# Kernel tuning notes

Hardware: AMD Instinct MI355X
Metric: run time of the kernel (lower is better)

Reference implementation:

```python
import jax, jax.numpy as jnp
import numpy as np

B, T, C = 2, 2048, 2048
N_HEAD = 16
N_KV = 4
HEAD = C // N_HEAD  # 128
GROUP = N_HEAD // N_KV


def setup_inputs() -> dict:
    key = jax.random.key(0)
    ks = jax.random.split(key, 5)
    s = 1.0 / np.sqrt(C)
    return {
        "x": jax.random.normal(ks[0], (B, T, C), dtype=jnp.float32),
        "Wq": jax.random.normal(ks[1], (C, C), dtype=jnp.float32) * s,
        "Wk": jax.random.normal(ks[2], (C, N_KV * HEAD), dtype=jnp.float32) * s,
        "Wv": jax.random.normal(ks[3], (C, N_KV * HEAD), dtype=jnp.float32) * s,
        "Wo": jax.random.normal(ks[4], (C, C), dtype=jnp.float32) * s,
    }


def reference(x, Wq, Wk, Wv, Wo):
    Bx, Tx, Cx = x.shape
    q = (x @ Wq).reshape(Bx, Tx, N_HEAD, HEAD).transpose(0, 2, 1, 3)  # (B,H,T,D)
    k = (x @ Wk).reshape(Bx, Tx, N_KV, HEAD).transpose(0, 2, 1, 3)    # (B,KV,T,D)
    v = (x @ Wv).reshape(Bx, Tx, N_KV, HEAD).transpose(0, 2, 1, 3)
    # expand kv heads to query heads (GQA): repeat each kv head GROUP times
    k = jnp.repeat(k, GROUP, axis=1)  # (B,H,T,D)
    v = jnp.repeat(v, GROUP, axis=1)
    scale = 1.0 / np.sqrt(HEAD).astype(np.float32)
    att = jnp.einsum("bhqd,bhkd->bhqk", q, k) * scale  # (B,H,T,T)
    causal = jnp.tril(jnp.ones((Tx, Tx), dtype=bool))
    att = jnp.where(causal[None, None], att, -jnp.inf)
    att = jax.nn.softmax(att, axis=-1)
    y = jnp.einsum("bhqk,bhkd->bhqd", att, v)  # (B,H,T,D)
    y = y.transpose(0, 2, 1, 3).reshape(Bx, Tx, Cx)
    return y @ Wo
```

## Files before the change

kernel.cpp:

```cpp
#include <hip/hip_runtime.h>
#include <cstdint>

typedef unsigned short u16;
typedef unsigned int u32;
typedef __attribute__((ext_vector_type(8))) __bf16 bf16x8;
typedef __attribute__((ext_vector_type(4))) float f32x4;
typedef __attribute__((ext_vector_type(4))) unsigned short u16x4;

#define AS1 __attribute__((address_space(1)))
#define AS3 __attribute__((address_space(3)))

__device__ __forceinline__ void gload16(const void* g, void* l) {
    __builtin_amdgcn_global_load_lds((AS1 void*)g, (AS3 void*)l, 16, 0, 0);
}

__device__ __forceinline__ u16 f2bf(float f) {
    return __builtin_bit_cast(u16, (__bf16)f);
}

__device__ __forceinline__ void store_c(u16* p, float v)   { *p = f2bf(v); }
__device__ __forceinline__ void store_c(float* p, float v) { *p = v; }

__global__ void prep(const float* __restrict__ x,
                     const float* __restrict__ Wq, const float* __restrict__ Wk,
                     const float* __restrict__ Wv, const float* __restrict__ Wo,
                     u16* __restrict__ xb, u16* __restrict__ Wt)
{
    const int bid = blockIdx.x;
    if (bid >= 10240) {
        int tid = threadIdx.y * 32 + threadIdx.x;
        size_t i = ((size_t)(bid - 10240) * 256 + tid) * 4;
        float4 v = *(const float4*)(x + i);
        u16x4 o = { f2bf(v.x), f2bf(v.y), f2bf(v.z), f2bf(v.w) };
        *(u16x4*)(xb + i) = o;
        return;
    }
    const float* src; u16* dst; int C, bx, by;
    if (bid < 4096)      { src = Wq; dst = Wt;                          C = 2048; bx = bid & 63; by = bid >> 6; }
    else if (bid < 5120) { src = Wk; dst = Wt + (size_t)2048 * 2048;    C = 512;  int i = bid - 4096; bx = i & 15; by = i >> 4; }
    else if (bid < 6144) { src = Wv; dst = Wt + (size_t)2560 * 2048;    C = 512;  int i = bid - 5120; bx = i & 15; by = i >> 4; }
    else                 { src = Wo; dst = Wt + (size_t)3072 * 2048;    C = 2048; int i = bid - 6144; bx = i & 63; by = i >> 6; }
    __shared__ float tile[32][33];
    int c0 = bx * 32, r0 = by * 32;
    int tx = threadIdx.x, ty = threadIdx.y;
#pragma unroll
    for (int i = 0; i < 32; i += 8)
        tile[ty + i][tx] = src[(size_t)(r0 + ty + i) * C + c0 + tx];
    __syncthreads();
#pragma unroll
    for (int i = 0; i < 32; i += 8)
        dst[(size_t)(c0 + ty + i) * 2048 + r0 + tx] = f2bf(tile[tx][ty + i]);
}

__global__ void vtrans(const u16* __restrict__ QKV, u16* __restrict__ VT) {
    __shared__ u16 tile[32][33];
    int b = blockIdx.z;
    int c0 = blockIdx.x * 32, r0 = blockIdx.y * 32;
    int tx = threadIdx.x, ty = threadIdx.y;
#pragma unroll
    for (int i = 0; i < 32; i += 8)
        tile[ty + i][tx] = QKV[(size_t)(b * 2048 + r0 + ty + i) * 3072 + 2560 + c0 + tx];
    __syncthreads();
#pragma unroll
    for (int i = 0; i < 32; i += 8)
        VT[(size_t)(b * 512 + c0 + ty + i) * 2048 + r0 + tx] = tile[tx][ty + i];
}

template <typename OT>
__global__ __launch_bounds__(256, 2) void gemm_bt(
    const u16* __restrict__ A, const u16* __restrict__ Bt,
    OT* __restrict__ C, int M, int N, int K)
{
    __shared__ u16 As[128 * 64];
    __shared__ u16 Bs[128 * 64];
    const int tid  = threadIdx.x;
    const int wave = tid >> 6, lane = tid & 63;
    const int quad = lane >> 4, l15 = lane & 15;
    const int bm0 = blockIdx.y * 128, bn0 = blockIdx.x * 128;
    const int wr = (wave >> 1) * 64, wc = (wave & 1) * 64;

    const f32x4 zero = {0.f, 0.f, 0.f, 0.f};
    f32x4 acc[4][4];
#pragma unroll
    for (int i = 0; i < 4; ++i)
#pragma unroll
        for (int j = 0; j < 4; ++j) acc[i][j] = zero;

    const int srow = lane >> 3;
    const int jsw  = ((lane & 7) ^ srow) * 8;

    for (int k0 = 0; k0 < K; k0 += 64) {
#pragma unroll
        for (int i = 0; i < 4; ++i) {
            int c = wave * 4 + i;
            gload16(A  + (size_t)(bm0 + c * 8 + srow) * K + k0 + jsw, As + c * 512);
            gload16(Bt + (size_t)(bn0 + c * 8 + srow) * K + k0 + jsw, Bs + c * 512);
        }
        __syncthreads();
#pragma unroll
        for (int ks = 0; ks < 2; ++ks) {
            bf16x8 a[4], b[4];
#pragma unroll
            for (int t = 0; t < 4; ++t) {
                int rd = ((ks * 4 + quad) ^ (l15 & 7)) * 8;
                a[t] = *(const bf16x8*)(As + (wr + t * 16 + l15) * 64 + rd);
                b[t] = *(const bf16x8*)(Bs + (wc + t * 16 + l15) * 64 + rd);
            }
#pragma unroll
            for (int i = 0; i < 4; ++i)
#pragma unroll
                for (int j = 0; j < 4; ++j)
                    acc[i][j] = __builtin_amdgcn_mfma_f32_16x16x32_bf16(a[i], b[j], acc[i][j], 0, 0, 0);
        }
        __syncthreads();
    }
#pragma unroll
    for (int i = 0; i < 4; ++i) {
        int grow = bm0 + wr + i * 16 + quad * 4;
#pragma unroll
        for (int j = 0; j < 4; ++j) {
            int gcol = bn0 + wc + j * 16 + l15;
#pragma unroll
            for (int r = 0; r < 4; ++r)
                store_c(&C[(size_t)(grow + r) * N + gcol], acc[i][j][r]);
        }
    }
}

__global__ __launch_bounds__(256, 2) void attn(
    const u16* __restrict__ QKV, const u16* __restrict__ VT, u16* __restrict__ Y)
{
    __shared__ u16 Ks[2][64 * 128];
    __shared__ u16 Vs[2][128 * 64];
    __shared__ u16 Ps[4][16 * 80];

    const int tid  = threadIdx.x;
    const int wave = tid >> 6, lane = tid & 63;
    const int quad = lane >> 4, l15 = lane & 15;
    const int pi = blockIdx.x;
    const int qtA = pi, qtB = 31 - pi;
    const int bh = blockIdx.y;
    const int b = bh >> 4, h = bh & 15, kv = h >> 2;

    const int myqt = (wave < 2) ? qtA : qtB;
    const int qbase = (wave & 1) * 32;
    const int q0 = myqt * 64 + qbase;

    bf16x8 aq[2][4];
#pragma unroll
    for (int mt = 0; mt < 2; ++mt) {
        const u16* qp = QKV + (size_t)(b * 2048 + q0 + mt * 16 + l15) * 3072 + h * 128 + quad * 8;
#pragma unroll
        for (int ks = 0; ks < 4; ++ks) aq[mt][ks] = *(const bf16x8*)(qp + ks * 32);
    }

    bf16x8 ones;
#pragma unroll
    for (int i = 0; i < 8; ++i) ones[i] = __builtin_bit_cast(__bf16, (u16)0x3F80);

    const f32x4 zero = {0.f, 0.f, 0.f, 0.f};
    f32x4 o[2][8], o8[2];
#pragma unroll
    for (int mt = 0; mt < 2; ++mt) {
#pragma unroll
        for (int i = 0; i < 8; ++i) o[mt][i] = zero;
        o8[mt] = zero;
    }

    const u16* Kbase = QKV + 2048 + kv * 128;
    const u16* Vbase = VT + (size_t)((b * 4 + kv) * 128) * 2048;
    u16* pw = &Ps[wave][0];

    const int kr = lane >> 4;
    const int vr = lane >> 3;
    const int vjs = ((lane & 7) ^ vr) * 8;

    auto stage = [&](int buf, int kt) {
#pragma unroll
        for (int i = 0; i < 4; ++i) {
            int ci = wave * 4 + i;
            int krow = ci * 4 + kr;
            int kjs = ((lane & 15) ^ (krow & 15)) * 8;
            gload16(Kbase + (size_t)(b * 2048 + kt * 64 + krow) * 3072 + kjs,
                    &Ks[buf][ci * 512]);
            int vrow = ci * 8 + vr;
            gload16(Vbase + (size_t)vrow * 2048 + kt * 64 + vjs, &Vs[buf][ci * 512]);
        }
    };

    const float c1 = 0.12752817f;
    const float c2 = 28.85390082f;

    stage(0, 0);
    __syncthreads();

    for (int kt = 0; kt <= qtB; ++kt) {
        const int cur = kt & 1;
        if (kt < qtB) stage(cur ^ 1, kt + 1);

        if (kt <= myqt) {
            const u16* Ksc = &Ks[cur][0];
            const u16* Vsc = &Vs[cur][0];

            f32x4 s[2][4];
#pragma unroll
            for (int mt = 0; mt < 2; ++mt)
#pragma unroll
                for (int i = 0; i < 4; ++i) s[mt][i] = zero;
#pragma unroll
            for (int ks = 0; ks < 4; ++ks)
#pragma unroll
                for (int kc = 0; kc < 4; ++kc) {
                    bf16x8 bk = *(const bf16x8*)(Ksc + (kc * 16 + l15) * 128 + (((ks * 4 + quad) ^ l15) * 8));
                    s[0][kc] = __builtin_amdgcn_mfma_f32_16x16x32_bf16(aq[0][ks], bk, s[0][kc], 0, 0, 0);
                    s[1][kc] = __builtin_amdgcn_mfma_f32_16x16x32_bf16(aq[1][ks], bk, s[1][kc], 0, 0, 0);
                }
            const bool diag = (kt == myqt);

#pragma unroll
            for (int mt = 0; mt < 2; ++mt) {
#pragma unroll
                for (int kc = 0; kc < 4; ++kc)
#pragma unroll
                    for (int r = 0; r < 4; ++r) {
                        float arg = fmaf(s[mt][kc][r], c1, -c2);
                        if (diag && (kc * 16 + l15) > (qbase + mt * 16 + quad * 4 + r)) arg = -10000.f;
                        float p = __builtin_amdgcn_exp2f(arg);
                        pw[(quad * 4 + r) * 80 + kc * 16 + l15] = f2bf(p);
                    }
                asm volatile("" ::: "memory");
#pragma unroll
                for (int ks2 = 0; ks2 < 2; ++ks2) {
                    bf16x8 pa = *(const bf16x8*)(pw + l15 * 80 + ks2 * 32 + quad * 8);
#pragma unroll
                    for (int d = 0; d < 8; ++d) {
                        bf16x8 bv = *(const bf16x8*)(Vsc + (d * 16 + l15) * 64 + (((ks2 * 4 + quad) ^ (l15 & 7)) * 8));
                        o[mt][d] = __builtin_amdgcn_mfma_f32_16x16x32_bf16(pa, bv, o[mt][d], 0, 0, 0);
                    }
                    o8[mt] = __builtin_amdgcn_mfma_f32_16x16x32_bf16(pa, ones, o8[mt], 0, 0, 0);
                }
                asm volatile("" ::: "memory");
            }
        }

        __syncthreads();
    }

#pragma unroll
    for (int mt = 0; mt < 2; ++mt) {
        float inv[4];
#pragma unroll
        for (int r = 0; r < 4; ++r) inv[r] = 1.0f / o8[mt][r];
#pragma unroll
        for (int d = 0; d < 8; ++d)
#pragma unroll
            for (int r = 0; r < 4; ++r)
                Y[(size_t)(b * 2048 + q0 + mt * 16 + quad * 4 + r) * 2048 + h * 128 + d * 16 + l15] =
                    f2bf(o[mt][d][r] * inv[r]);
    }
}

extern "C" void kernel_launch(void* const* d_in, const int* in_sizes, int n_in,
                              void* d_out, int out_size, void* d_ws, size_t ws_size,
                              hipStream_t stream)
{
    const float* x  = (const float*)d_in[0];
    const float* Wq = (const float*)d_in[1];
    const float* Wk = (const float*)d_in[2];
    const float* Wv = (const float*)d_in[3];
    const float* Wo = (const float*)d_in[4];
    float* out = (float*)d_out;

    char* ws = (char*)d_ws;
    u16* xb   = (u16*)ws; ws += (size_t)4096 * 2048 * 2;
    u16* Wt   = (u16*)ws; ws += (size_t)5120 * 2048 * 2;
    u16* QKVb = (u16*)ws; ws += (size_t)4096 * 3072 * 2;
    u16* VT   = (u16*)ws;
    u16* Y    = xb;
    u16* WoT  = Wt + (size_t)3072 * 2048;

    prep<<<18432, dim3(32, 8, 1), 0, stream>>>(x, Wq, Wk, Wv, Wo, xb, Wt);

    gemm_bt<u16><<<dim3(24, 32, 1), 256, 0, stream>>>(xb, Wt, QKVb, 4096, 3072, 2048);

    vtrans<<<dim3(16, 64, 2), dim3(32, 8, 1), 0, stream>>>(QKVb, VT);

    attn<<<dim3(16, 32, 1), 256, 0, stream>>>(QKVb, VT, Y);

    gemm_bt<float><<<dim3(16, 32, 1), 256, 0, stream>>>(Y, WoT, out, 4096, 2048, 2048);
}
```

Measured before the change: 283.9 us.

## Process two GQA heads per block on one query tile, swizzle P buffer

The attention kernel now gives each block a single 64-row query tile and two query heads that share one KV head, with each wave owning 16 rows. Before, a block paired two query tiles for load balance, which left half the waves idle on later key tiles. Each staged K/V tile is now reused by two heads' MFMAs, and every wave stays busy through the whole loop. Heavy tiles are launched first to soften the uneven causal work per block. The P scratch buffer moves to an XOR-swizzled 64-wide layout to cut LDS bank conflicts, at the cost of losing the paired-tile balancing.

Result: faster. 273.5 us (-3.6%).

```diff
diff --git a/kernel.cpp b/kernel.cpp
--- a/kernel.cpp
+++ b/kernel.cpp
@@ -132,26 +132,23 @@
 {
     __shared__ u16 Ks[2][64 * 128];
     __shared__ u16 Vs[2][128 * 64];
-    __shared__ u16 Ps[4][16 * 80];
+    __shared__ u16 Ps[4][2][16 * 64];
 
     const int tid  = threadIdx.x;
     const int wave = tid >> 6, lane = tid & 63;
     const int quad = lane >> 4, l15 = lane & 15;
-    const int pi = blockIdx.x;
-    const int qtA = pi, qtB = 31 - pi;
-    const int bh = blockIdx.y;
-    const int b = bh >> 4, h = bh & 15, kv = h >> 2;
-
-    const int myqt = (wave < 2) ? qtA : qtB;
-    const int qbase = (wave & 1) * 32;
-    const int q0 = myqt * 64 + qbase;
+    const int qt = 31 - (int)blockIdx.y;
+    const int hb = blockIdx.x;
+    const int b = hb >> 3, kv = (hb >> 1) & 3, hp = hb & 1;
+    const int h0 = kv * 4 + hp * 2;
+    const int q0 = qt * 64 + wave * 16;
 
     bf16x8 aq[2][4];
 #pragma unroll
-    for (int mt = 0; mt < 2; ++mt) {
-        const u16* qp = QKV + (size_t)(b * 2048 + q0 + mt * 16 + l15) * 3072 + h * 128 + quad * 8;
-#pragma unroll
-        for (int ks = 0; ks < 4; ++ks) aq[mt][ks] = *(const bf16x8*)(qp + ks * 32);
+    for (int hh = 0; hh < 2; ++hh) {
+        const u16* qp = QKV + (size_t)(b * 2048 + q0 + l15) * 3072 + (h0 + hh) * 128 + quad * 8;
+#pragma unroll
+        for (int ks = 0; ks < 4; ++ks) aq[hh][ks] = *(const bf16x8*)(qp + ks * 32);
     }
 
     bf16x8 ones;
@@ -161,15 +158,14 @@
     const f32x4 zero = {0.f, 0.f, 0.f, 0.f};
     f32x4 o[2][8], o8[2];
 #pragma unroll
-    for (int mt = 0; mt < 2; ++mt) {
-#pragma unroll
-        for (int i = 0; i < 8; ++i) o[mt][i] = zero;
-        o8[mt] = zero;
+    for (int hh = 0; hh < 2; ++hh) {
+#pragma unroll
+        for (int i = 0; i < 8; ++i) o[hh][i] = zero;
+        o8[hh] = zero;
     }
 
     const u16* Kbase = QKV + 2048 + kv * 128;
     const u16* Vbase = VT + (size_t)((b * 4 + kv) * 128) * 2048;
-    u16* pw = &Ps[wave][0];
 
     const int kr = lane >> 4;
     const int vr = lane >> 3;
@@ -194,69 +190,74 @@
     stage(0, 0);
     __syncthreads();
 
-    for (int kt = 0; kt <= qtB; ++kt) {
+    for (int kt = 0; kt <= qt; ++kt) {
         const int cur = kt & 1;
-        if (kt < qtB) stage(cur ^ 1, kt + 1);
-
-        if (kt <= myqt) {
-            const u16* Ksc = &Ks[cur][0];
-            const u16* Vsc = &Vs[cur][0];
-
-            f32x4 s[2][4];
-#pragma unroll
-            for (int mt = 0; mt < 2; ++mt)
-#pragma unroll
-                for (int i = 0; i < 4; ++i) s[mt][i] = zero;
-#pragma unroll
-            for (int ks = 0; ks < 4; ++ks)
-#pragma unroll
-                for (int kc = 0; kc < 4; ++kc) {
-                    bf16x8 bk = *(const bf16x8*)(Ksc + (kc * 16 + l15) * 128 + (((ks * 4 + quad) ^ l15) * 8));
-                    s[0][kc] = __builtin_amdgcn_mfma_f32_16x16x32_bf16(aq[0][ks], bk, s[0][kc], 0, 0, 0);
-                    s[1][kc] = __builtin_amdgcn_mfma_f32_16x16x32_bf16(aq[1][ks], bk, s[1][kc], 0, 0, 0);
+        if (kt < qt) stage(cur ^ 1, kt + 1);
+
+        const u16* Ksc = &Ks[cur][0];
+        const u16* Vsc = &Vs[cur][0];
+
+        f32x4 s[2][4];
+#pragma unroll
+        for (int hh = 0; hh < 2; ++hh)
+#pragma unroll
+            for (int i = 0; i < 4; ++i) s[hh][i] = zero;
+#pragma unroll
+        for (int ks = 0; ks < 4; ++ks)
+#pragma unroll
+            for (int kc = 0; kc < 4; ++kc) {
+                bf16x8 bk = *(const bf16x8*)(Ksc + (kc * 16 + l15) * 128 + (((ks * 4 + quad) ^ l15) * 8));
+                s[0][kc] = __builtin_amdgcn_mfma_f32_16x16x32_bf16(aq[0][ks], bk, s[0][kc], 0, 0, 0);
+                s[1][kc] = __builtin_amdgcn_mfma_f32_16x16x32_bf16(aq[1][ks], bk, s[1][kc], 0, 0, 0);
+            }
+        const bool diag = (kt == qt);
+
+#pragma unroll
+        for (int hh = 0; hh < 2; ++hh) {
+            u16* pw = &Ps[wave][hh][0];
+#pragma unroll
+            for (int kc = 0; kc < 4; ++kc)
+#pragma unroll
+                for (int r = 0; r < 4; ++r) {
+                    float arg = fmaf(s[hh][kc][r], c1, -c2);
+                    if (diag && (kc * 16 + l15) > (wave * 16 + quad * 4 + r)) arg = -10000.f;
+                    float p = __builtin_amdgcn_exp2f(arg);
+                    int row = quad * 4 + r;
+                    int chunk = (kc * 2 + (l15 >> 3)) ^ (row & 7);
+                    pw[row * 64 + chunk * 8 + (l15 & 7)] = f2bf(p);
                 }
-            const bool diag = (kt == myqt);
-
-#pragma unroll
-            for (int mt = 0; mt < 2; ++mt) {
-#pragma unroll
-                for (int kc = 0; kc < 4; ++kc)
-#pragma unroll
-                    for (int r = 0; r < 4; ++r) {
-                        float arg = fmaf(s[mt][kc][r], c1, -c2);
-                        if (diag && (kc * 16 + l15) > (qbase + mt * 16 + quad * 4 + r)) arg = -10000.f;
-                        float p = __builtin_amdgcn_exp2f(arg);
-                        pw[(quad * 4 + r) * 80 + kc * 16 + l15] = f2bf(p);
-                    }
-                asm volatile("" ::: "memory");
-#pragma unroll
-                for (int ks2 = 0; ks2 < 2; ++ks2) {
-                    bf16x8 pa = *(const bf16x8*)(pw + l15 * 80 + ks2 * 32 + quad * 8);
-#pragma unroll
-                    for (int d = 0; d < 8; ++d) {
-                        bf16x8 bv = *(const bf16x8*)(Vsc + (d * 16 + l15) * 64 + (((ks2 * 4 + quad) ^ (l15 & 7)) * 8));
-                        o[mt][d] = __builtin_amdgcn_mfma_f32_16x16x32_bf16(pa, bv, o[mt][d], 0, 0, 0);
-                    }
-                    o8[mt] = __builtin_amdgcn_mfma_f32_16x16x32_bf16(pa, ones, o8[mt], 0, 0, 0);
-                }
-                asm volatile("" ::: "memory");
+        }
+        asm volatile("" ::: "memory");
+
+#pragma unroll
+        for (int ks2 = 0; ks2 < 2; ++ks2) {
+            const int prd = ((ks2 * 4 + quad) ^ (l15 & 7)) * 8;
+            bf16x8 pa0 = *(const bf16x8*)(&Ps[wave][0][0] + l15 * 64 + prd);
+            bf16x8 pa1 = *(const bf16x8*)(&Ps[wave][1][0] + l15 * 64 + prd);
+#pragma unroll
+            for (int d = 0; d < 8; ++d) {
+                bf16x8 bv = *(const bf16x8*)(Vsc + (d * 16 + l15) * 64 + prd);
+                o[0][d] = __builtin_amdgcn_mfma_f32_16x16x32_bf16(pa0, bv, o[0][d], 0, 0, 0);
+                o[1][d] = __builtin_amdgcn_mfma_f32_16x16x32_bf16(pa1, bv, o[1][d], 0, 0, 0);
             }
+            o8[0] = __builtin_amdgcn_mfma_f32_16x16x32_bf16(pa0, ones, o8[0], 0, 0, 0);
+            o8[1] = __builtin_amdgcn_mfma_f32_16x16x32_bf16(pa1, ones, o8[1], 0, 0, 0);
         }
 
         __syncthreads();
     }
 
 #pragma unroll
-    for (int mt = 0; mt < 2; ++mt) {
+    for (int hh = 0; hh < 2; ++hh) {
         float inv[4];
 #pragma unroll
-        for (int r = 0; r < 4; ++r) inv[r] = 1.0f / o8[mt][r];
+        for (int r = 0; r < 4; ++r) inv[r] = 1.0f / o8[hh][r];
 #pragma unroll
         for (int d = 0; d < 8; ++d)
 #pragma unroll
             for (int r = 0; r < 4; ++r)
-                Y[(size_t)(b * 2048 + q0 + mt * 16 + quad * 4 + r) * 2048 + h * 128 + d * 16 + l15] =
-                    f2bf(o[mt][d][r] * inv[r]);
+                Y[(size_t)(b * 2048 + q0 + quad * 4 + r) * 2048 + (h0 + hh) * 128 + d * 16 + l15] =
+                    f2bf(o[hh][d][r] * inv[r]);
     }
 }
 
```
